# Kernel optimization log

Hardware: AMD Instinct MI355X
Metric: run time of the kernel (lower is better)

Reference implementation:

```python
import jax, jax.numpy as jnp
import numpy as np

B, F, U, H1, H2 = 2048, 256, 64, 64, 32
E = F + 1  # attention embed dim = num_inputs + 1


def setup_inputs() -> dict:
    key = jax.random.key(0)
    ks = jax.random.split(key, 14)
    s = lambda fan: 1.0 / np.sqrt(fan)
    inp = {
        "x": jax.random.normal(ks[0], (B, F), jnp.float32),
        # stacked per-feature FeatureNN params (Linear(1,U) -> Linear(U,H1) -> Linear(H1,H2) -> Linear(H2,1))
        "w1": jax.random.normal(ks[1], (F, U), jnp.float32) * s(1),
        "b1": jnp.zeros((F, U), jnp.float32),
        "w2": jax.random.normal(ks[2], (F, U, H1), jnp.float32) * s(U),
        "b2": jnp.zeros((F, H1), jnp.float32),
        "w3": jax.random.normal(ks[3], (F, H1, H2), jnp.float32) * s(H1),
        "b3": jnp.zeros((F, H2), jnp.float32),
        "w4": jax.random.normal(ks[4], (F, H2), jnp.float32) * s(H2),
        "b4": jnp.zeros((F,), jnp.float32),
        # MultiheadAttention(E, 1) params: packed qkv in_proj + out_proj
        "in_w": jax.random.normal(ks[5], (3 * E, E), jnp.float32) * s(E),
        "in_b": jnp.zeros((3 * E,), jnp.float32),
        "out_w": jax.random.normal(ks[6], (E, E), jnp.float32) * s(E),
        "out_b": jnp.zeros((E,), jnp.float32),
        "bias": jnp.zeros((1,), jnp.float32),
    }
    return inp


def _attention(x, in_w, in_b, out_w, out_b):
    # x: [B, F]; build [B, F, E] = concat(one-hot feature index, value)
    b = x.shape[0]
    eye = jnp.eye(F, dtype=x.dtype)
    xa = jnp.concatenate([jnp.broadcast_to(eye, (b, F, F)), x[:, :, None]], axis=-1)  # [B,F,E]
    qkv = jnp.einsum("bse,fe->bsf", xa, in_w) + in_b  # [B,F,3E]
    q, k, v = jnp.split(qkv, 3, axis=-1)
    scores = jnp.einsum("bqe,bke->bqk", q, k) / jnp.sqrt(jnp.asarray(E, x.dtype))
    attn = jax.nn.softmax(scores, axis=-1)
    ctx = jnp.einsum("bqk,bke->bqe", attn, v)
    out = jnp.einsum("bqe,fe->bqf", ctx, out_w) + out_b  # out_proj
    return out[:, :, -1]  # keep only the value channel -> [B, F]


def _feature_nns(x, w1, b1, w2, b2, w3, b3, w4, b4):
    # x: [B, F] -> per-feature independent MLPs, batched across features
    h = jax.nn.relu(x[:, :, None] * w1[None] + b1[None])          # [B,F,U]
    h = jax.nn.relu(jnp.einsum("bfu,fuh->bfh", h, w2) + b2[None])  # [B,F,H1]
    h = jax.nn.relu(jnp.einsum("bfh,fhg->bfg", h, w3) + b3[None])  # [B,F,H2]
    return jnp.einsum("bfg,fg->bf", h, w4) + b4[None]              # [B,F]


def reference(x, w1, b1, w2, b2, w3, b3, w4, b4, in_w, in_b, out_w, out_b, bias):
    xa = _attention(x, in_w, in_b, out_w, out_b)                   # att_before_flag=True
    fo = _feature_nns(xa, w1, b1, w2, b2, w3, b3, w4, b4)          # dropout is identity (p=0 / eval)
    out = jnp.sum(fo, axis=-1) + bias                              # [B] + bias -> [B]
    return (out, fo)
```

## Files before the change

### kernel.cpp

```cpp
#include <hip/hip_runtime.h>

#define BB 2048
#define FF 256
#define EE 257
#define UU 64
#define HH1 64
#define HH2 32

#define SC 0.089992807f

typedef __attribute__((ext_vector_type(8))) short short8;
typedef __attribute__((ext_vector_type(4))) float f32x4;
typedef __attribute__((ext_vector_type(4))) unsigned u32x4;
typedef __attribute__((ext_vector_type(2))) unsigned u32x2;

#define MF(a, b, c) __builtin_amdgcn_mfma_f32_16x16x32_bf16(a, b, c, 0, 0, 0)
#define EXP2(x) __builtin_amdgcn_exp2f(x)

__device__ inline unsigned cvt_pk(float a, float b) {
    unsigned r;
    asm("v_cvt_pk_bf16_f32 %0, %1, %2" : "=v"(r) : "v"(a), "v"(b));
    return r;
}
struct HiLo { unsigned hi, lo; };
__device__ inline HiLo split2(float a, float b) {
    HiLo r;
    r.hi = cvt_pk(a, b);
    float ha = __builtin_bit_cast(float, r.hi << 16);
    float hb = __builtin_bit_cast(float, r.hi & 0xFFFF0000u);
    r.lo = cvt_pk(a - ha, b - hb);
    return r;
}
__device__ inline f32x4 splat4(float v) { f32x4 r; r[0]=v; r[1]=v; r[2]=v; r[3]=v; return r; }

__global__ __launch_bounds__(256) void k_prep(const float* __restrict__ in_w,
                                              const float* __restrict__ in_b,
                                              const float* __restrict__ out_w,
                                              const float* __restrict__ out_b,
                                              const float* __restrict__ w2,
                                              const float* __restrict__ w3,
                                              float* __restrict__ mt,
                                              float* __restrict__ uv, float* __restrict__ wgf,
                                              float* __restrict__ sc,
                                              short* __restrict__ w2s, short* __restrict__ w3s) {
    const int blk = blockIdx.x;
    const int t = threadIdx.x;
    __shared__ float red[4][256];
    __shared__ float s0[EE + 3];
    __shared__ float s1[EE + 3];
    if (blk < 256) {
        const int ki = blk;
        for (int j = t; j < EE; j += 256) {
            s0[j] = in_w[(EE + j) * EE + ki] + in_b[EE + j];
            s1[j] = in_b[j];
        }
        __syncthreads();
        const int w = t >> 6, l = t & 63;
        const int j0 = (w * EE) >> 2, j1 = ((w + 1) * EE) >> 2;
        float acc[4] = {0.f, 0.f, 0.f, 0.f};
#pragma unroll 4
        for (int j = j0; j < j1; ++j) {
            float ak = s0[j];
            float bj = s1[j];
#pragma unroll
            for (int g = 0; g < 4; ++g) {
                float aq = in_w[j * EE + l + 64 * g] + bj;
                acc[g] = fmaf(aq, ak, acc[g]);
            }
        }
#pragma unroll
        for (int g = 0; g < 4; ++g) red[w][l + 64 * g] = acc[g];
        __syncthreads();
        {
            float s = red[0][t] + red[1][t] + red[2][t] + red[3][t];
            mt[(ki >> 1) * 512 + t * 2 + (ki & 1)] = s * SC;
        }
    } else if (blk < 512) {
        const int f = blk - 256;
        const int l = t & 63, q = t >> 6;
        const int lr = l & 15, lq = l >> 4;
        const float* w2f = w2 + f * (UU * HH1);
        const float* w3f = w3 + f * (HH1 * HH2);
        short* o2 = w2s + f * 8192;
        short* o3 = w3s + f * 4096;
#pragma unroll
        for (int kb = 0; kb < 2; ++kb) {
            float v[8];
#pragma unroll
            for (int j = 0; j < 8; ++j) v[j] = w2f[(kb * 32 + lq * 8 + j) * HH1 + q * 16 + lr];
            u32x4 hi, lo;
#pragma unroll
            for (int p = 0; p < 4; ++p) {
                HiLo s = split2(v[2 * p], v[2 * p + 1]);
                hi[p] = s.hi; lo[p] = s.lo;
            }
            *(short8*)(o2 + ((0 * 2 + kb) * 4 + q) * 512 + l * 8) = __builtin_bit_cast(short8, hi);
            *(short8*)(o2 + ((1 * 2 + kb) * 4 + q) * 512 + l * 8) = __builtin_bit_cast(short8, lo);
        }
        {
            const int kb = q & 1, ct = q >> 1;
            float v[8];
#pragma unroll
            for (int j = 0; j < 8; ++j) v[j] = w3f[(kb * 32 + lq * 8 + j) * HH2 + ct * 16 + lr];
            u32x4 hi, lo;
#pragma unroll
            for (int p = 0; p < 4; ++p) {
                HiLo s = split2(v[2 * p], v[2 * p + 1]);
                hi[p] = s.hi; lo[p] = s.lo;
            }
            *(short8*)(o3 + ((0 * 2 + kb) * 2 + ct) * 512 + l * 8) = __builtin_bit_cast(short8, hi);
            *(short8*)(o3 + ((1 * 2 + kb) * 2 + ct) * 512 + l * 8) = __builtin_bit_cast(short8, lo);
        }
    } else if (blk < 515) {
        const int which = blk - 512;
        for (int j = t; j < EE; j += 256) {
            if (which == 0)      { s0[j] = in_w[(EE + j) * EE + FF];    s1[j] = in_b[j]; }
            else if (which == 1) { s0[j] = in_w[j * EE + FF];           s1[j] = in_b[EE + j]; }
            else                 { s0[j] = out_w[(EE - 1) * EE + j];    s1[j] = in_b[2 * EE + j]; }
        }
        __syncthreads();
        const int w = t >> 6, l = t & 63;
        const int j0 = (w * EE) >> 2, j1 = ((w + 1) * EE) >> 2;
        const int rowbase = which * EE;
        float acc[4] = {0.f, 0.f, 0.f, 0.f};
#pragma unroll 4
        for (int j = j0; j < j1; ++j) {
            float sk = s0[j];
            float bj = s1[j];
#pragma unroll
            for (int g = 0; g < 4; ++g) {
                float av = in_w[(rowbase + j) * EE + l + 64 * g] + bj;
                acc[g] = fmaf(av, sk, acc[g]);
            }
        }
#pragma unroll
        for (int g = 0; g < 4; ++g) red[w][l + 64 * g] = acc[g];
        __syncthreads();
        {
            float s = red[0][t] + red[1][t] + red[2][t] + red[3][t];
            if (which == 0)      uv[t]          = s * SC;
            else if (which == 1) wgf[2 * t]     = s * SC;
            else                 wgf[2 * t + 1] = s;
        }
    } else {
        const int j = t;
        float cq = in_w[j * EE + FF];
        float ck = in_w[(EE + j) * EE + FF];
        float cv = in_w[(2 * EE + j) * EE + FF];
        float rj = out_w[(EE - 1) * EE + j];
        float pa = cq * ck, pb = cv * rj;
        if (t == 0) {
            const int j2 = 256;
            pa += in_w[j2 * EE + FF] * in_w[(EE + j2) * EE + FF];
            pb += in_w[(2 * EE + j2) * EE + FF] * out_w[(EE - 1) * EE + j2];
        }
#pragma unroll
        for (int o = 32; o > 0; o >>= 1) {
            pa += __shfl_down(pa, o, 64);
            pb += __shfl_down(pb, o, 64);
        }
        if ((t & 63) == 0) { red[0][t >> 6] = pa; red[1][t >> 6] = pb; }
        __syncthreads();
        if (t == 0) {
            pa = red[0][0] + red[0][1] + red[0][2] + red[0][3];
            pb = red[1][0] + red[1][1] + red[1][2] + red[1][3];
            sc[0] = pa * SC;
            sc[1] = pb;
            sc[2] = out_b[EE - 1];
        }
    }
}

__global__ __launch_bounds__(256) void k2_attn(const float* __restrict__ x,
                                               const float2* __restrict__ mt2,
                                               const float* __restrict__ uv,
                                               const float* __restrict__ wg,
                                               const float* __restrict__ sc,
                                               float* __restrict__ xa) {
    const int qi = threadIdx.x;
    const int b0 = blockIdx.x * 2;
    __shared__ __align__(16) float xs0[FF];
    __shared__ __align__(16) float xs1[FF];
    __shared__ __align__(16) float wgs[2 * FF];
    xs0[qi] = x[b0 * FF + qi];
    xs1[qi] = x[(b0 + 1) * FF + qi];
    *(float2*)&wgs[2 * qi] = *(const float2*)&wg[2 * qi];
    const float alpha_s = sc[0], beta = sc[1], ob = sc[2];
    const float uq = uv[qi];
    __syncthreads();
    const float xq0 = xs0[qi];
    const float xq1 = xs1[qi];
    const float a0 = fmaf(alpha_s, xq0, uq);
    const float a1 = fmaf(alpha_s, xq1, uq);
    float le0 = 0.f, le1 = 0.f, p0 = 0.f, p1 = 0.f, q0 = 0.f, q1 = 0.f;
#pragma unroll 8
    for (int kp = 0; kp < FF / 2; ++kp) {
        const float2 m   = mt2[kp * FF + qi];
        const f32x4 wgk  = *(const f32x4*)&wgs[4 * kp];
        const float2 xk0 = *(const float2*)&xs0[2 * kp];
        const float2 xk1 = *(const float2*)&xs1[2 * kp];
        float e;
        e = EXP2(fmaf(xk0.x, a0, fmaf(wgk[0], xq0, m.x))); le0 += e; p0 = fmaf(e, wgk[1], p0); q0 = fmaf(e, xk0.x, q0);
        e = EXP2(fmaf(xk0.y, a0, fmaf(wgk[2], xq0, m.y))); le0 += e; p0 = fmaf(e, wgk[3], p0); q0 = fmaf(e, xk0.y, q0);
        e = EXP2(fmaf(xk1.x, a1, fmaf(wgk[0], xq1, m.x))); le1 += e; p1 = fmaf(e, wgk[1], p1); q1 = fmaf(e, xk1.x, q1);
        e = EXP2(fmaf(xk1.y, a1, fmaf(wgk[2], xq1, m.y))); le1 += e; p1 = fmaf(e, wgk[3], p1); q1 = fmaf(e, xk1.y, q1);
    }
    xa[b0 * FF + qi]       = (p0 + beta * q0) / le0 + ob;
    xa[(b0 + 1) * FF + qi] = (p1 + beta * q1) / le1 + ob;
}

__global__ __launch_bounds__(256, 3) void k3_fnn(const float* xa_in,
                                                 const float* __restrict__ w1,
                                                 const float* __restrict__ b1,
                                                 const float* __restrict__ b2,
                                                 const float* __restrict__ b3,
                                                 const float* __restrict__ w4,
                                                 const float* __restrict__ b4,
                                                 const short* __restrict__ w2s,
                                                 const short* __restrict__ w3s,
                                                 float* fo) {
    const int f   = blockIdx.x & 255;
    const int rq  = blockIdx.x >> 8;
    const int tid = threadIdx.x;
    const int wv  = tid >> 6;
    const int l   = tid & 63;
    const int lr  = l & 15;
    const int lq  = l >> 4;

    const float* w1f = w1 + f * UU;
    const float* b1f = b1 + f * UU;
    const float* b2f = b2 + f * HH1;
    const float* b3f = b3 + f * HH2;
    const float* w4f = w4 + f * HH2;
    const short* w2sf = w2s + f * 8192;
    const short* w3sf = w3s + f * 4096;

    const float B3s0 = b3f[lr], B3s1 = b3f[16 + lr];
    const float w4v0 = w4f[lr], w4v1 = w4f[16 + lr];
    const float b4v  = b4[f];

    short8 W3h[2][2], W3l[2][2];
#pragma unroll
    for (int ct = 0; ct < 2; ++ct)
#pragma unroll
        for (int kb = 0; kb < 2; ++kb) {
            W3h[ct][kb] = *(const short8*)(w3sf + ((0 * 2 + kb) * 2 + ct) * 512 + l * 8);
            W3l[ct][kb] = *(const short8*)(w3sf + ((1 * 2 + kb) * 2 + ct) * 512 + l * 8);
        }

    __shared__ __align__(16) short lds2[4][32][2][64];
    short* myl = &lds2[wv][0][0][0];

    const int cstart = (rq * 64) / 3;
    const int cend   = ((rq + 1) * 64) / 3;
    for (int ch = cstart + wv; ch < cend; ch += 4) {
        const int rows0 = ch * 32;

        const float xv0 = xa_in[(rows0 + lr) * FF + f];
        const float xv1 = xa_in[(rows0 + 16 + lr) * FF + f];
        short8 Bh[2][2], Bl[2][2];
#pragma unroll
        for (int kb = 0; kb < 2; ++kb) {
            f32x4 wA = *(const f32x4*)(w1f + kb * 32 + lq * 8);
            f32x4 wB = *(const f32x4*)(w1f + kb * 32 + lq * 8 + 4);
            f32x4 bA = *(const f32x4*)(b1f + kb * 32 + lq * 8);
            f32x4 bB = *(const f32x4*)(b1f + kb * 32 + lq * 8 + 4);
#pragma unroll
            for (int rbt = 0; rbt < 2; ++rbt) {
                const float xv = rbt ? xv1 : xv0;
                float h[8];
#pragma unroll
                for (int j = 0; j < 4; ++j) h[j]     = fmaxf(fmaf(xv, wA[j], bA[j]), 0.f);
#pragma unroll
                for (int j = 0; j < 4; ++j) h[4 + j] = fmaxf(fmaf(xv, wB[j], bB[j]), 0.f);
                u32x4 bh, bl;
#pragma unroll
                for (int p = 0; p < 4; ++p) {
                    HiLo s = split2(h[2 * p], h[2 * p + 1]);
                    bh[p] = s.hi; bl[p] = s.lo;
                }
                Bh[rbt][kb] = __builtin_bit_cast(short8, bh);
                Bl[rbt][kb] = __builtin_bit_cast(short8, bl);
            }
        }

#pragma unroll
        for (int ht = 0; ht < 4; ++ht) {
            const short8 W2h0 = *(const short8*)(w2sf + (0 * 4 + ht) * 512 + l * 8);
            const short8 W2h1 = *(const short8*)(w2sf + (1 * 4 + ht) * 512 + l * 8);
            const short8 W2l0 = *(const short8*)(w2sf + (2 * 4 + ht) * 512 + l * 8);
            const short8 W2l1 = *(const short8*)(w2sf + (3 * 4 + ht) * 512 + l * 8);
            const f32x4 binit = *(const f32x4*)(b2f + ht * 16 + lq * 4);
#pragma unroll
            for (int rbt = 0; rbt < 2; ++rbt) {
                f32x4 acc = binit;
                acc = MF(W2h0, Bh[rbt][0], acc);
                acc = MF(W2h1, Bh[rbt][1], acc);
                acc = MF(W2h0, Bl[rbt][0], acc);
                acc = MF(W2h1, Bl[rbt][1], acc);
                acc = MF(W2l0, Bh[rbt][0], acc);
                acc = MF(W2l1, Bh[rbt][1], acc);
                const int row = rbt * 16 + lr;
                const int swz = (row & 7) << 3;
                const int hb  = (ht * 16 + lq * 4) ^ swz;
                float v0 = fmaxf(acc[0], 0.f), v1 = fmaxf(acc[1], 0.f);
                float v2 = fmaxf(acc[2], 0.f), v3 = fmaxf(acc[3], 0.f);
                HiLo p0 = split2(v0, v1);
                HiLo p1 = split2(v2, v3);
                u32x2 hiw, low;
                hiw[0] = p0.hi; hiw[1] = p1.hi;
                low[0] = p0.lo; low[1] = p1.lo;
                *(u32x2*)(myl + row * 128 + hb)      = hiw;
                *(u32x2*)(myl + row * 128 + 64 + hb) = low;
            }
        }

#pragma unroll
        for (int rbt = 0; rbt < 2; ++rbt) {
            const int row = rbt * 16 + lr;
            const int swz = (row & 7) << 3;
            const short8 Ah0 = *(const short8*)(myl + row * 128 + ((0  + lq * 8) ^ swz));
            const short8 Ah1 = *(const short8*)(myl + row * 128 + ((32 + lq * 8) ^ swz));
            const short8 Al0 = *(const short8*)(myl + row * 128 + 64 + ((0  + lq * 8) ^ swz));
            const short8 Al1 = *(const short8*)(myl + row * 128 + 64 + ((32 + lq * 8) ^ swz));
            f32x4 a0 = splat4(B3s0);
            f32x4 a1 = splat4(B3s1);
            a0 = MF(Ah0, W3h[0][0], a0); a0 = MF(Ah1, W3h[0][1], a0);
            a0 = MF(Ah0, W3l[0][0], a0); a0 = MF(Ah1, W3l[0][1], a0);
            a0 = MF(Al0, W3h[0][0], a0); a0 = MF(Al1, W3h[0][1], a0);
            a1 = MF(Ah0, W3h[1][0], a1); a1 = MF(Ah1, W3h[1][1], a1);
            a1 = MF(Ah0, W3l[1][0], a1); a1 = MF(Ah1, W3l[1][1], a1);
            a1 = MF(Al0, W3h[1][0], a1); a1 = MF(Al1, W3h[1][1], a1);
            float sr0 = fmaf(fmaxf(a0[0], 0.f), w4v0, fmaxf(a1[0], 0.f) * w4v1);
            float sr1 = fmaf(fmaxf(a0[1], 0.f), w4v0, fmaxf(a1[1], 0.f) * w4v1);
            float sr2 = fmaf(fmaxf(a0[2], 0.f), w4v0, fmaxf(a1[2], 0.f) * w4v1);
            float sr3 = fmaf(fmaxf(a0[3], 0.f), w4v0, fmaxf(a1[3], 0.f) * w4v1);
#pragma unroll
            for (int m = 1; m < 16; m <<= 1) {
                sr0 += __shfl_xor(sr0, m, 64);
                sr1 += __shfl_xor(sr1, m, 64);
                sr2 += __shfl_xor(sr2, m, 64);
                sr3 += __shfl_xor(sr3, m, 64);
            }
            if (lr == 0) {
                const int rb = rows0 + rbt * 16 + lq * 4;
                fo[(rb + 0) * FF + f] = sr0 + b4v;
                fo[(rb + 1) * FF + f] = sr1 + b4v;
                fo[(rb + 2) * FF + f] = sr2 + b4v;
                fo[(rb + 3) * FF + f] = sr3 + b4v;
            }
        }
    }
}

__global__ __launch_bounds__(64) void k4_sum(const float* __restrict__ fo,
                                             const float* __restrict__ bias,
                                             float* __restrict__ out) {
    const int b = blockIdx.x;
    const int t = threadIdx.x;
    const float* r = fo + b * FF;
    float s = r[t] + r[t + 64] + r[t + 128] + r[t + 192];
#pragma unroll
    for (int o = 32; o > 0; o >>= 1) s += __shfl_down(s, o, 64);
    if (t == 0) out[b] = s + bias[0];
}

extern "C" void kernel_launch(void* const* d_in, const int* in_sizes, int n_in,
                              void* d_out, int out_size, void* d_ws, size_t ws_size,
                              hipStream_t stream) {
    const float* x    = (const float*)d_in[0];
    const float* w1   = (const float*)d_in[1];
    const float* b1   = (const float*)d_in[2];
    const float* w2   = (const float*)d_in[3];
    const float* b2   = (const float*)d_in[4];
    const float* w3   = (const float*)d_in[5];
    const float* b3   = (const float*)d_in[6];
    const float* w4   = (const float*)d_in[7];
    const float* b4   = (const float*)d_in[8];
    const float* in_w = (const float*)d_in[9];
    const float* in_b = (const float*)d_in[10];
    const float* out_w= (const float*)d_in[11];
    const float* out_b= (const float*)d_in[12];
    const float* bias = (const float*)d_in[13];

    float* out = (float*)d_out;
    float* fo  = out + BB;
    float* ws  = (float*)d_ws;
    float* mt  = ws;
    float* uvp = ws + 65536;
    float* wgp = ws + 65792;
    float* scp = ws + 66304;
    short* w2s = (short*)(ws + 66560);
    short* w3s = w2s + 256 * 8192;

    k_prep<<<516, 256, 0, stream>>>(in_w, in_b, out_w, out_b, w2, w3,
                                    mt, uvp, wgp, scp, w2s, w3s);
    k2_attn<<<BB / 2, 256, 0, stream>>>(x, (const float2*)mt, uvp, wgp, scp, fo);
    k3_fnn<<<FF * 3, 256, 0, stream>>>(fo, w1, b1, b2, b3, w4, b4, w2s, w3s, fo);
    k4_sum<<<BB, 64, 0, stream>>>(fo, bias, out);
}
```

Measured before the change: 72.73 us.

## Hoist W2 fragments into registers and prefetch next chunk inputs in FNN kernel

The per-feature MLP kernel now loads all layer-2 weight fragments into registers once per block instead of reloading them for every chunk. Each wave handles a fixed four chunks of 32 rows in a fully unrolled loop that prefetches the next chunk's inputs while computing the current one. The grid changes from 3 to 4 blocks per feature so the work splits evenly. Keeping 16 extra short8 fragments in registers raises register pressure, which may reduce occupancy or cause spills under the launch bound of 3 blocks per SM. The kernel's parameter order is also shuffled.

```diff
diff --git a/kernel.cpp b/kernel.cpp
--- a/kernel.cpp
+++ b/kernel.cpp
@@ -210,12 +210,12 @@
 }
 
 __global__ __launch_bounds__(256, 3) void k3_fnn(const float* xa_in,
-                                                 const float* __restrict__ w1,
-                                                 const float* __restrict__ b1,
                                                  const float* __restrict__ b2,
                                                  const float* __restrict__ b3,
                                                  const float* __restrict__ w4,
                                                  const float* __restrict__ b4,
+                                                 const float* __restrict__ w1,
+                                                 const float* __restrict__ b1,
                                                  const short* __restrict__ w2s,
                                                  const short* __restrict__ w3s,
                                                  float* fo) {
@@ -239,6 +239,14 @@
     const float w4v0 = w4f[lr], w4v1 = w4f[16 + lr];
     const float b4v  = b4[f];
 
+    short8 W2h[4][2], W2l[4][2];
+#pragma unroll
+    for (int ht = 0; ht < 4; ++ht) {
+        W2h[ht][0] = *(const short8*)(w2sf + (0 * 4 + ht) * 512 + l * 8);
+        W2h[ht][1] = *(const short8*)(w2sf + (1 * 4 + ht) * 512 + l * 8);
+        W2l[ht][0] = *(const short8*)(w2sf + (2 * 4 + ht) * 512 + l * 8);
+        W2l[ht][1] = *(const short8*)(w2sf + (3 * 4 + ht) * 512 + l * 8);
+    }
     short8 W3h[2][2], W3l[2][2];
 #pragma unroll
     for (int ct = 0; ct < 2; ++ct)
@@ -251,13 +259,17 @@
     __shared__ __align__(16) short lds2[4][32][2][64];
     short* myl = &lds2[wv][0][0][0];
 
-    const int cstart = (rq * 64) / 3;
-    const int cend   = ((rq + 1) * 64) / 3;
-    for (int ch = cstart + wv; ch < cend; ch += 4) {
-        const int rows0 = ch * 32;
-
-        const float xv0 = xa_in[(rows0 + lr) * FF + f];
-        const float xv1 = xa_in[(rows0 + 16 + lr) * FF + f];
+    int rows0 = (rq * 16 + wv * 4) * 32;
+    float xv0 = xa_in[(rows0 + lr) * FF + f];
+    float xv1 = xa_in[(rows0 + 16 + lr) * FF + f];
+#pragma unroll
+    for (int c = 0; c < 4; ++c) {
+        float nxv0 = 0.f, nxv1 = 0.f;
+        if (c < 3) {
+            nxv0 = xa_in[(rows0 + 32 + lr) * FF + f];
+            nxv1 = xa_in[(rows0 + 48 + lr) * FF + f];
+        }
+
         short8 Bh[2][2], Bl[2][2];
 #pragma unroll
         for (int kb = 0; kb < 2; ++kb) {
@@ -286,20 +298,16 @@
 
 #pragma unroll
         for (int ht = 0; ht < 4; ++ht) {
-            const short8 W2h0 = *(const short8*)(w2sf + (0 * 4 + ht) * 512 + l * 8);
-            const short8 W2h1 = *(const short8*)(w2sf + (1 * 4 + ht) * 512 + l * 8);
-            const short8 W2l0 = *(const short8*)(w2sf + (2 * 4 + ht) * 512 + l * 8);
-            const short8 W2l1 = *(const short8*)(w2sf + (3 * 4 + ht) * 512 + l * 8);
             const f32x4 binit = *(const f32x4*)(b2f + ht * 16 + lq * 4);
 #pragma unroll
             for (int rbt = 0; rbt < 2; ++rbt) {
                 f32x4 acc = binit;
-                acc = MF(W2h0, Bh[rbt][0], acc);
-                acc = MF(W2h1, Bh[rbt][1], acc);
-                acc = MF(W2h0, Bl[rbt][0], acc);
-                acc = MF(W2h1, Bl[rbt][1], acc);
-                acc = MF(W2l0, Bh[rbt][0], acc);
-                acc = MF(W2l1, Bh[rbt][1], acc);
+                acc = MF(W2h[ht][0], Bh[rbt][0], acc);
+                acc = MF(W2h[ht][1], Bh[rbt][1], acc);
+                acc = MF(W2h[ht][0], Bl[rbt][0], acc);
+                acc = MF(W2h[ht][1], Bl[rbt][1], acc);
+                acc = MF(W2l[ht][0], Bh[rbt][0], acc);
+                acc = MF(W2l[ht][1], Bh[rbt][1], acc);
                 const int row = rbt * 16 + lr;
                 const int swz = (row & 7) << 3;
                 const int hb  = (ht * 16 + lq * 4) ^ swz;
@@ -350,6 +358,8 @@
                 fo[(rb + 3) * FF + f] = sr3 + b4v;
             }
         }
+
+        xv0 = nxv0; xv1 = nxv1; rows0 += 32;
     }
 }
 
@@ -396,6 +406,6 @@
     k_prep<<<516, 256, 0, stream>>>(in_w, in_b, out_w, out_b, w2, w3,
                                     mt, uvp, wgp, scp, w2s, w3s);
     k2_attn<<<BB / 2, 256, 0, stream>>>(x, (const float2*)mt, uvp, wgp, scp, fo);
-    k3_fnn<<<FF * 3, 256, 0, stream>>>(fo, w1, b1, b2, b3, w4, b4, w2s, w3s, fo);
+    k3_fnn<<<FF * 4, 256, 0, stream>>>(fo, b2, b3, w4, b4, w1, b1, w2s, w3s, fo);
     k4_sum<<<BB, 64, 0, stream>>>(fo, bias, out);
 }
```

After: 90.44 us. 1.24x slower.
